# Kernel optimization log

Hardware: AMD Instinct MI355X
Metric: run time of the kernel (lower is better)

Reference implementation:

```python
import jax, jax.numpy as jnp
import numpy as np

N = 262144   # query points
M = 4096     # boundary points
D = 128      # d_model (m)
H = 4        # num_heads
HD = D // H  # head_dim = 32
L = 3        # num_layers
PI = float(np.pi)


def multi_feature_encoding(x):
    # x: [T, 2] -> [T, 30]; 15 fixed feature maps, hstacked
    feats = [
        x,
        x ** 2,
        (x - 1.5) ** 2,
        (x - 4.5) ** 2,
        jax.nn.sigmoid(x),
        jax.nn.sigmoid(x - 1.5),
        jax.nn.sigmoid(x - 4.5),
        x - 1.5,
        x - 4.5,
        jnp.sin(PI * x),
        jnp.cos(PI * x),
        jnp.sin(PI * x * 0.25),
        jnp.cos(PI * x * 0.25),
        jnp.sin(PI * x * 0.5),
        jnp.cos(PI * x * 0.5),
    ]
    return jnp.concatenate(feats, axis=-1)


def pos_encode(x, w, b):
    # w: [30, D], b: [D]
    return jnp.sin(multi_feature_encoding(x) @ w + b)


def setup_inputs() -> dict:
    key = jax.random.key(0)
    ks = jax.random.split(key, 24)
    s = 0.05

    def p(k, shape):
        return jax.random.normal(k, shape, dtype=jnp.float32) * s

    return {
        "query_pts": jax.random.normal(ks[0], (N, 2), dtype=jnp.float32),
        "boundary_pts": jax.random.normal(ks[1], (M, 2), dtype=jnp.float32),
        # positional encoders (query / boundary)
        "pe_w": p(ks[2], (30, D)), "pe_b": p(ks[3], (D,)),
        "bpe_w": p(ks[4], (30, D)), "bpe_b": p(ks[5], (D,)),
        # per-layer per-head q/k/v projections, stacked: [L, H, D, HD]
        "Wq": p(ks[6], (L, H, D, HD)), "bq": p(ks[7], (L, H, HD)),
        "Wk": p(ks[8], (L, H, D, HD)), "bk": p(ks[9], (L, H, HD)),
        "Wv": p(ks[10], (L, H, D, HD)), "bv": p(ks[11], (L, H, HD)),
        # attention out proj and FFN (two D->D linears) per layer
        "Wo": p(ks[12], (L, D, D)), "bo": p(ks[13], (L, D)),
        "W1": p(ks[14], (L, D, D)), "b1": p(ks[15], (L, D)),
        "W2": p(ks[16], (L, D, D)), "b2": p(ks[17], (L, D)),
        # final projector: D -> D//2 -> 3
        "pw1": p(ks[18], (D, D // 2)), "pb1": p(ks[19], (D // 2,)),
        "pw2": p(ks[20], (D // 2, 3)), "pb2": p(ks[21], (3,)),
    }


def reference(query_pts, boundary_pts, pe_w, pe_b, bpe_w, bpe_b,
              Wq, bq, Wk, bk, Wv, bv, Wo, bo, W1, b1, W2, b2,
              pw1, pb1, pw2, pb2):
    h = pos_encode(query_pts, pe_w, pe_b)[None]        # [1, N, D]
    b_enc = pos_encode(boundary_pts, bpe_w, bpe_b)[None]  # [1, M, D]

    for l in range(L):
        # batched per-head projections (equivalent to the per-head Linear loop)
        qh = jnp.einsum('btd,hde->bhte', h, Wq[l]) + bq[l][None, :, None, :]
        kh = jnp.einsum('btd,hde->bhte', b_enc, Wk[l]) + bk[l][None, :, None, :]
        vh = jnp.einsum('btd,hde->bhte', b_enc, Wv[l]) + bv[l][None, :, None, :]
        qh = qh ** 2  # squared feature map
        kh = kh ** 2
        kv_sum = jnp.einsum('bhnd,bhne->bhde', kh, vh)          # [1,H,HD,HD]
        z = 1.0 / (jnp.einsum('bhnd,bhd->bhn', qh, kh.sum(axis=2)) + 1e-6)
        attn = jnp.einsum('bhnd,bhde,bhn->bhne', qh, kv_sum, z)  # [1,H,N,HD]
        attn = attn.transpose(0, 2, 1, 3).reshape(1, -1, D)      # [1,N,D]
        attn = attn @ Wo[l] + bo[l]
        x = h + attn
        ff = jax.nn.gelu(x @ W1[l] + b1[l], approximate=False) @ W2[l] + b2[l]
        h = x + ff

    out = jax.nn.gelu(h @ pw1 + pb1, approximate=False) @ pw2 + pb2  # [1,N,3]
    return out[0]  # squeeze(0) -> [N, 3]
```

## Files before the change

### kernel.cpp

```cpp
#include <hip/hip_runtime.h>
#include <hip/hip_bf16.h>

__device__ __forceinline__ float b2f(unsigned short u) {
    return __uint_as_float(((unsigned)u) << 16);
}
__device__ __forceinline__ unsigned short f2b(float f) {
    __hip_bfloat16 h = __float2bfloat16(f);
    return *reinterpret_cast<unsigned short*>(&h);
}
__device__ __forceinline__ unsigned pk_bf16(float lo, float hi) {
    unsigned r;
    asm("v_cvt_pk_bf16_f32 %0, %1, %2" : "=v"(r) : "v"(lo), "v"(hi));
    return r;
}
__device__ __forceinline__ float exp2_hw(float x) {
    float r;
    asm("v_exp_f32 %0, %1" : "=v"(r) : "v"(x));
    return r;
}
__device__ __forceinline__ float sigm(float v) {
    return 1.f / (1.f + __expf(-v));
}
__device__ __forceinline__ float gelu_l(float x) {
    float x2 = x * x;
    float y  = x * __builtin_fmaf(0.10294535f, x2, 2.3022137f);
    float e  = exp2_hw(y);
    float r  = __builtin_amdgcn_rcpf(e + 1.f);
    return __builtin_fmaf(-x, r, x);
}

typedef __attribute__((ext_vector_type(8))) short s8v;
typedef __attribute__((ext_vector_type(4))) float f4v;

#define MFMA_BF16 __builtin_amdgcn_mfma_f32_16x16x32_bf16

__device__ __forceinline__ s8v mkfrag(unsigned a, unsigned b, unsigned c, unsigned d) {
    union { unsigned u[4]; s8v v; } x;
    x.u[0] = a; x.u[1] = b; x.u[2] = c; x.u[3] = d;
    return x.v;
}

__device__ __forceinline__ int fmap(int s) {
    return (s & ~31) | (((s >> 2) & 3) << 3) | (((s >> 4) & 1) << 2) | (s & 3);
}
__device__ __forceinline__ int swz_q(int q) {
    return q ^ (((q >> 7) & 7) << 3);
}

__device__ __forceinline__ void make_feats(const unsigned short* __restrict__ qpts,
                                           int r, float* __restrict__ f) {
    unsigned pq = *(const unsigned*)(qpts + (size_t)r * 2);
    float x0 = b2f((unsigned short)(pq & 0xffff));
    float x1 = b2f((unsigned short)(pq >> 16));
    const float PI = 3.14159265358979323846f;
    float a0 = x0 - 1.5f, a1 = x1 - 1.5f, c0 = x0 - 4.5f, c1 = x1 - 4.5f;
    f[0] = x0;        f[1] = x1;
    f[2] = x0 * x0;   f[3] = x1 * x1;
    f[4] = a0 * a0;   f[5] = a1 * a1;
    f[6] = c0 * c0;   f[7] = c1 * c1;
    f[8] = sigm(x0);  f[9] = sigm(x1);
    f[10] = sigm(a0); f[11] = sigm(a1);
    f[12] = sigm(c0); f[13] = sigm(c1);
    f[14] = a0;       f[15] = a1;
    f[16] = c0;       f[17] = c1;
    f[18] = __sinf(PI * x0);          f[19] = __sinf(PI * x1);
    f[20] = __cosf(PI * x0);          f[21] = __cosf(PI * x1);
    f[22] = __sinf(PI * 0.25f * x0);  f[23] = __sinf(PI * 0.25f * x1);
    f[24] = __cosf(PI * 0.25f * x0);  f[25] = __cosf(PI * 0.25f * x1);
    f[26] = __sinf(PI * 0.5f * x0);   f[27] = __sinf(PI * 0.5f * x1);
    f[28] = __cosf(PI * 0.5f * x0);   f[29] = __cosf(PI * 0.5f * x1);
}

__device__ __forceinline__ void feats8(unsigned pq, int qd, float* __restrict__ f8) {
    float x0 = b2f((unsigned short)(pq & 0xffff));
    float x1 = b2f((unsigned short)(pq >> 16));
    const float PI = 3.14159265358979323846f;
    float a0 = x0 - 1.5f, a1 = x1 - 1.5f, c0 = x0 - 4.5f, c1 = x1 - 4.5f;
    if (qd == 0) {
        f8[0] = x0;      f8[1] = x1;
        f8[2] = x0 * x0; f8[3] = x1 * x1;
        f8[4] = a0 * a0; f8[5] = a1 * a1;
        f8[6] = c0 * c0; f8[7] = c1 * c1;
    } else if (qd == 1) {
        f8[0] = sigm(x0); f8[1] = sigm(x1);
        f8[2] = sigm(a0); f8[3] = sigm(a1);
        f8[4] = sigm(c0); f8[5] = sigm(c1);
        f8[6] = a0;       f8[7] = a1;
    } else if (qd == 2) {
        f8[0] = c0; f8[1] = c1;
        f8[2] = __sinf(PI * x0);          f8[3] = __sinf(PI * x1);
        f8[4] = __cosf(PI * x0);          f8[5] = __cosf(PI * x1);
        f8[6] = __sinf(PI * 0.25f * x0);  f8[7] = __sinf(PI * 0.25f * x1);
    } else {
        f8[0] = __cosf(PI * 0.25f * x0);  f8[1] = __cosf(PI * 0.25f * x1);
        f8[2] = __sinf(PI * 0.5f * x0);   f8[3] = __sinf(PI * 0.5f * x1);
        f8[4] = __cosf(PI * 0.5f * x0);   f8[5] = __cosf(PI * 0.5f * x1);
        f8[6] = 0.f;                      f8[7] = 0.f;
    }
}

struct ConvArgs {
    const void* p[22];
    int off[23];
};

__global__ __launch_bounds__(256) void convert_kernel(
    ConvArgs a, const unsigned short* __restrict__ pe_w_raw,
    int* __restrict__ flag, unsigned short* __restrict__ canon, int total)
{
    __shared__ int cnt;
    if (threadIdx.x == 0) cnt = 0;
    __syncthreads();
    float v = b2f(pe_w_raw[threadIdx.x * 2]);
    if (!(fabsf(v) < 1.0f)) atomicAdd(&cnt, 1);
    __syncthreads();
    int isf32 = (cnt >= 16) ? 1 : 0;
    if (blockIdx.x == 0 && threadIdx.x == 0) *flag = isf32;

    int g = blockIdx.x * 256 + threadIdx.x;
    if (g >= total) return;
    int s = 0;
    #pragma unroll
    for (int i = 1; i < 23; i++) s += (g >= a.off[i]) ? 1 : 0;
    int local = g - a.off[s];
    unsigned short r;
    if (isf32) r = f2b(((const float*)a.p[s])[local]);
    else       r = ((const unsigned short*)a.p[s])[local];
    canon[g] = r;
}

__global__ __launch_bounds__(256) void encode_kernel(
    const unsigned short* __restrict__ pts,
    const unsigned short* __restrict__ w,
    const unsigned short* __restrict__ b,
    float* __restrict__ out)
{
    __shared__ __align__(16) float wsm[30 * 128];
    __shared__ float bs[128];
    int t = threadIdx.x;
    for (int i = t; i < 30 * 128; i += 256) wsm[i] = b2f(w[i]);
    if (t < 128) bs[t] = b2f(b[t]);
    __syncthreads();

    int r = blockIdx.x * 8 + (t >> 5);
    int j = t & 31;
    float f[30];
    make_feats(pts, r, f);
    float s0 = bs[j * 4 + 0], s1 = bs[j * 4 + 1], s2 = bs[j * 4 + 2], s3 = bs[j * 4 + 3];
    #pragma unroll
    for (int ff = 0; ff < 30; ff++) {
        float4 wv = *(const float4*)&wsm[ff * 128 + j * 4];
        float fv = f[ff];
        s0 += fv * wv.x; s1 += fv * wv.y; s2 += fv * wv.z; s3 += fv * wv.w;
    }
    *(float4*)&out[(size_t)r * 128 + j * 4] =
        make_float4(__sinf(s0), __sinf(s1), __sinf(s2), __sinf(s3));
}

__global__ __launch_bounds__(256) void khvh_kernel(
    const float* __restrict__ benc,
    const unsigned short* __restrict__ Wk, const unsigned short* __restrict__ bk,
    const unsigned short* __restrict__ Wv, const unsigned short* __restrict__ bv,
    float* __restrict__ kh, float* __restrict__ vh, float* __restrict__ kvz)
{
    int g = blockIdx.x * 256 + threadIdx.x;
    if (g < 12672) kvz[g] = 0.f;
    int lh = g >> 17;
    int rem = g & 131071;
    int m = rem >> 5;
    int dd = rem & 31;
    const unsigned short* wk = Wk + lh * 4096 + dd;
    const unsigned short* wv = Wv + lh * 4096 + dd;
    const float* br = benc + (size_t)m * 128;
    float ka = 0.f, va = 0.f;
    #pragma unroll 8
    for (int c = 0; c < 128; c++) {
        float bb = br[c];
        ka += bb * b2f(wk[c * 32]);
        va += bb * b2f(wv[c * 32]);
    }
    ka += b2f(bk[lh * 32 + dd]); ka = ka * ka;
    va += b2f(bv[lh * 32 + dd]);
    kh[g] = ka; vh[g] = va;
}

__global__ __launch_bounds__(1024) void kvred_kernel(
    const float* __restrict__ kh, const float* __restrict__ vh,
    float* __restrict__ kvsum, float* __restrict__ ksum)
{
    __shared__ float khs[1024];
    __shared__ float vhs[1024];
    int t = threadIdx.x;
    int lh = blockIdx.x >> 3;
    int part = blockIdx.x & 7;
    int dd = t >> 5, ee = t & 31;
    float kva = 0.f, ksa = 0.f;
    for (int ch = 0; ch < 16; ch++) {
        int base = lh * 131072 + (part * 16 + ch) * 1024;
        khs[t] = kh[base + t];
        vhs[t] = vh[base + t];
        __syncthreads();
        #pragma unroll
        for (int i = 0; i < 32; i++) {
            float kk = khs[i * 32 + dd];
            kva += kk * vhs[i * 32 + ee];
            ksa += kk;
        }
        __syncthreads();
    }
    atomicAdd(&kvsum[lh * 1024 + dd * 32 + ee], kva);
    if (ee == 0) atomicAdd(&ksum[lh * 32 + dd], ksa);
}

__global__ __launch_bounds__(256) void prep_kernel(
    const unsigned short* __restrict__ Wq, const unsigned short* __restrict__ W1,
    const unsigned short* __restrict__ W2, const unsigned short* __restrict__ pw1,
    const float* __restrict__ kvs, const float* __restrict__ kss,
    const unsigned short* __restrict__ Wo, const unsigned short* __restrict__ pe_w,
    unsigned short* __restrict__ wqT, unsigned short* __restrict__ w1T,
    unsigned short* __restrict__ w2T, unsigned short* __restrict__ pw1T,
    unsigned short* __restrict__ waT, unsigned short* __restrict__ ksT,
    unsigned short* __restrict__ pweT)
{
    int g = blockIdx.x * 256 + threadIdx.x;
    if (g < 49152) {
        int l = g >> 14, q = swz_q(g & 16383), n = q >> 7, k = q & 127;
        int na = fmap(n);
        wqT[g] = Wq[((l * 4 + (na >> 5)) * 128 + k) * 32 + (na & 31)];
    } else if (g < 98304) {
        int q0 = g - 49152; int l = q0 >> 14, q = swz_q(q0 & 16383), n = q >> 7, k = q & 127;
        w1T[q0] = W1[(l * 128 + k) * 128 + fmap(n)];
    } else if (g < 147456) {
        int q0 = g - 98304; int l = q0 >> 14, q = swz_q(q0 & 16383), n = q >> 7, k = q & 127;
        w2T[q0] = W2[(l * 128 + k) * 128 + fmap(n)];
    } else if (g < 155648) {
        int q0 = g - 147456; int q = swz_q(q0), n = q >> 7, k = q & 127;
        pw1T[q0] = pw1[k * 64 + n];
    } else if (g < 204800) {
        int q0 = g - 155648; int l = q0 >> 14, q = swz_q(q0 & 16383), n = q >> 7, k = q & 127;
        int na = fmap(n);
        int hk = k >> 5, dk = k & 31;
        const float* kvp = kvs + (l * 4 + hk) * 1024 + dk * 32;
        const unsigned short* wop = Wo + (size_t)(l * 128 + hk * 32) * 128 + na;
        float s = 0.f;
        #pragma unroll 8
        for (int j = 0; j < 32; j++) s += kvp[j] * b2f(wop[j * 128]);
        waT[q0] = f2b(s);
    } else if (g < 210944) {
        int q = g - 204800; int l = q >> 11, r = q & 2047, n = r >> 7, k = r & 127;
        unsigned short v = 0;
        if (n < 4 && (k >> 5) == n) v = f2b(kss[(l * 4 + n) * 32 + (k & 31)]);
        ksT[q] = v;
    } else if (g < 215040) {
        int q = g - 210944; int n = q >> 5, k = q & 31;
        pweT[q] = (k < 30) ? pe_w[k * 128 + fmap(n)] : (unsigned short)0;
    }
}


template<int ITERS>
__device__ __forceinline__ void stage_gll(const unsigned short* __restrict__ g,
                                          unsigned short* __restrict__ lbase,
                                          int wvi, int ln) {
    const char* gp = (const char*)g + wvi * 1024 + ln * 16;
    char* lp = (char*)lbase + wvi * 1024;
    #pragma unroll
    for (int i = 0; i < ITERS; i++) {
        __builtin_amdgcn_global_load_lds(
            (const __attribute__((address_space(1))) unsigned int*)(gp + i * 4096),
            (__attribute__((address_space(3))) unsigned int*)(lp + i * 4096),
            16, 0, 0);
    }
}

__device__ __forceinline__ s8v wfrag(const unsigned short* __restrict__ wb,
                                     int nt, int k, int l16, int qd) {
    int lin = (nt << 12) + (l16 << 8) + (k << 6) + (qd << 4);
    return *(const s8v*)((const char*)wb + (lin ^ ((l16 & 7) << 4)));
}

#define MM_BODY(WB, EPI...) do {                                              \
    s8v bf0[4], bf1[4];                                                       \
    _Pragma("unroll")                                                         \
    for (int _s = 0; _s < 4; _s++) {                                          \
        bf0[_s] = mkfrag(pkd[0][2*_s][0], pkd[0][2*_s][1],                    \
                         pkd[0][2*_s+1][0], pkd[0][2*_s+1][1]);               \
        bf1[_s] = mkfrag(pkd[1][2*_s][0], pkd[1][2*_s][1],                    \
                         pkd[1][2*_s+1][0], pkd[1][2*_s+1][1]);               \
    }                                                                         \
    _Pragma("unroll")                                                         \
    for (int _p = 0; _p < 4; _p++) {                                          \
        f4v _x0 = {0.f,0.f,0.f,0.f}, _x1 = _x0, _y0 = _x0, _y1 = _x0;         \
        _Pragma("unroll")                                                     \
        for (int _k = 0; _k < 4; _k++) {                                      \
            s8v _wa = wfrag(WB, _p * 2,     _k, l16, qd);                     \
            s8v _wb = wfrag(WB, _p * 2 + 1, _k, l16, qd);                     \
            _x0 = MFMA_BF16(_wa, bf0[_k], _x0, 0, 0, 0);                      \
            _x1 = MFMA_BF16(_wa, bf1[_k], _x1, 0, 0, 0);                      \
            _y0 = MFMA_BF16(_wb, bf0[_k], _y0, 0, 0, 0);                      \
            _y1 = MFMA_BF16(_wb, bf1[_k], _y1, 0, 0, 0);                      \
        }                                                                     \
        { const int nt = _p * 2;     const int tile = 0; const f4v x = _x0; EPI } \
        { const int nt = _p * 2;     const int tile = 1; const f4v x = _x1; EPI } \
        { const int nt = _p * 2 + 1; const int tile = 0; const f4v x = _y0; EPI } \
        { const int nt = _p * 2 + 1; const int tile = 1; const f4v x = _y1; EPI } \
    }                                                                         \
} while (0)

#define CBDEF int cb = ((nt >> 1) << 5) + (qd << 3) + ((nt & 1) << 2)

__global__ __launch_bounds__(256) void mega_kernel(
    const unsigned short* __restrict__ qpts,
    const unsigned short* __restrict__ pweT,
    const unsigned short* __restrict__ pe_b,
    const unsigned short* __restrict__ wqT,
    const unsigned short* __restrict__ waT,
    const unsigned short* __restrict__ ksT,
    const unsigned short* __restrict__ w1T,
    const unsigned short* __restrict__ w2T,
    const unsigned short* __restrict__ bq,
    const unsigned short* __restrict__ bo,
    const unsigned short* __restrict__ b1,
    const unsigned short* __restrict__ b2,
    const unsigned short* __restrict__ pw1T,
    const unsigned short* __restrict__ pb1,
    const unsigned short* __restrict__ pw2,
    const unsigned short* __restrict__ pb2,
    void* __restrict__ outv, const int* __restrict__ flag)
{
    __shared__ __align__(16) unsigned short wbuf[2][16384];
    __shared__ __align__(16) float biasAll[12 * 128];
    __shared__ __align__(16) float pebs[128];
    __shared__ __align__(16) float pb1s[64];
    __shared__ __align__(16) float w2s4[256];
    __shared__ float pb2s[3];

    int t = threadIdx.x;
    int wvi = t >> 6, ln = t & 63, qd = ln >> 4, l16 = ln & 15;
    int row0 = blockIdx.x * 128;
    int rA0 = wvi * 32 + l16;
    unsigned short* wb0 = &wbuf[0][0];
    unsigned short* wb1 = &wbuf[1][0];

    stage_gll<8>(wqT, wb0, wvi, ln);

    for (int i = t; i < 1536; i += 256) {
        int l = i >> 9, rem = i & 511, which = rem >> 7, c = rem & 127;
        const unsigned short* bsrc = (which == 0) ? bq : (which == 1) ? bo
                                   : (which == 2) ? b1 : b2;
        biasAll[i] = b2f(bsrc[l * 128 + c]);
    }
    if (t < 128) pebs[t] = b2f(pe_b[t]);
    if (t < 64)  pb1s[t] = b2f(pb1[t]);
    if (t < 64) {
        w2s4[t * 4 + 0] = b2f(pw2[t * 3 + 0]);
        w2s4[t * 4 + 1] = b2f(pw2[t * 3 + 1]);
        w2s4[t * 4 + 2] = b2f(pw2[t * 3 + 2]);
        w2s4[t * 4 + 3] = 0.f;
    }
    if (t < 3) pb2s[t] = b2f(pb2[t]);
    __syncthreads();

    stage_gll<8>(waT, wb1, wvi, ln);

    unsigned pkd[2][8][2];
    float hres[2][8][4];

    {
        unsigned pq0 = *(const unsigned*)(qpts + (size_t)(row0 + rA0) * 2);
        unsigned pq1 = *(const unsigned*)(qpts + (size_t)(row0 + rA0 + 16) * 2);
        s8v ae0, ae1;
        {
            float f8[8]; feats8(pq0, qd, f8);
            unsigned* au = (unsigned*)&ae0;
            #pragma unroll
            for (int jj = 0; jj < 4; jj++) au[jj] = pk_bf16(f8[2 * jj], f8[2 * jj + 1]);
        }
        {
            float f8[8]; feats8(pq1, qd, f8);
            unsigned* au = (unsigned*)&ae1;
            #pragma unroll
            for (int jj = 0; jj < 4; jj++) au[jj] = pk_bf16(f8[2 * jj], f8[2 * jj + 1]);
        }
        const unsigned short* pb = pweT + l16 * 32 + qd * 8;
        #pragma unroll
        for (int nt = 0; nt < 8; nt++) {
            s8v aw = *(const s8v*)(pb + nt * 512);
            f4v x0 = {0.f, 0.f, 0.f, 0.f}, x1 = {0.f, 0.f, 0.f, 0.f};
            x0 = MFMA_BF16(aw, ae0, x0, 0, 0, 0);
            x1 = MFMA_BF16(aw, ae1, x1, 0, 0, 0);
            CBDEF;
            float4 bb = *(const float4*)&pebs[cb];
            float h0 = __sinf(x0[0] + bb.x), h1 = __sinf(x0[1] + bb.y);
            float h2 = __sinf(x0[2] + bb.z), h3 = __sinf(x0[3] + bb.w);
            hres[0][nt][0] = h0; hres[0][nt][1] = h1;
            hres[0][nt][2] = h2; hres[0][nt][3] = h3;
            pkd[0][nt][0] = pk_bf16(h0, h1);
            pkd[0][nt][1] = pk_bf16(h2, h3);
            float g0 = __sinf(x1[0] + bb.x), g1 = __sinf(x1[1] + bb.y);
            float g2 = __sinf(x1[2] + bb.z), g3 = __sinf(x1[3] + bb.w);
            hres[1][nt][0] = g0; hres[1][nt][1] = g1;
            hres[1][nt][2] = g2; hres[1][nt][3] = g3;
            pkd[1][nt][0] = pk_bf16(g0, g1);
            pkd[1][nt][1] = pk_bf16(g2, g3);
        }
    }

    for (int l = 0; l < 3; l++) {
        const float* bql = &biasAll[(l * 4 + 0) * 128];
        const float* bol = &biasAll[(l * 4 + 1) * 128];
        const float* b1l = &biasAll[(l * 4 + 2) * 128];
        const float* b2l = &biasAll[(l * 4 + 3) * 128];

        s8v kf[4];
        {
            const unsigned short* kb = ksT + l * 2048 + l16 * 128 + qd * 8;
            #pragma unroll
            for (int ks = 0; ks < 4; ks++) kf[ks] = *(const s8v*)(kb + ks * 32);
        }

        MM_BODY(wb0, {
            CBDEF;
            float4 bb = *(const float4*)&bql[cb];
            float v0 = x[0] + bb.x, v1 = x[1] + bb.y;
            float v2 = x[2] + bb.z, v3 = x[3] + bb.w;
            pkd[tile][nt][0] = pk_bf16(v0 * v0, v1 * v1);
            pkd[tile][nt][1] = pk_bf16(v2 * v2, v3 * v3);
        });
        __syncthreads();
        stage_gll<8>(w1T + l * 16384, wb0, wvi, ln);

        #pragma unroll
        for (int tile = 0; tile < 2; tile++) {
            f4v d = {0.f, 0.f, 0.f, 0.f};
            #pragma unroll
            for (int ks = 0; ks < 4; ks++) {
                s8v b = mkfrag(pkd[tile][2 * ks][0], pkd[tile][2 * ks][1],
                               pkd[tile][2 * ks + 1][0], pkd[tile][2 * ks + 1][1]);
                d = MFMA_BF16(kf[ks], b, d, 0, 0, 0);
            }
            #pragma unroll
            for (int ks = 0; ks < 4; ks++) {
                float z = 1.f / (__shfl(d[ks], l16) + 1e-6f);
                #pragma unroll
                for (int h2 = 0; h2 < 2; h2++) {
                    #pragma unroll
                    for (int j = 0; j < 2; j++) {
                        unsigned w = pkd[tile][2 * ks + h2][j];
                        float lo = __uint_as_float(w << 16) * z;
                        float hi = __uint_as_float(w & 0xffff0000u) * z;
                        pkd[tile][2 * ks + h2][j] = pk_bf16(lo, hi);
                    }
                }
            }
        }

        MM_BODY(wb1, {
            CBDEF;
            float4 bb = *(const float4*)&bol[cb];
            float v0 = hres[tile][nt][0] + x[0] + bb.x;
            float v1 = hres[tile][nt][1] + x[1] + bb.y;
            float v2 = hres[tile][nt][2] + x[2] + bb.z;
            float v3 = hres[tile][nt][3] + x[3] + bb.w;
            hres[tile][nt][0] = v0; hres[tile][nt][1] = v1;
            hres[tile][nt][2] = v2; hres[tile][nt][3] = v3;
            pkd[tile][nt][0] = pk_bf16(v0, v1);
            pkd[tile][nt][1] = pk_bf16(v2, v3);
        });
        __syncthreads();
        stage_gll<8>(w2T + l * 16384, wb1, wvi, ln);

        MM_BODY(wb0, {
            CBDEF;
            float4 bb = *(const float4*)&b1l[cb];
            float g0 = gelu_l(x[0] + bb.x), g1 = gelu_l(x[1] + bb.y);
            float g2 = gelu_l(x[2] + bb.z), g3 = gelu_l(x[3] + bb.w);
            pkd[tile][nt][0] = pk_bf16(g0, g1);
            pkd[tile][nt][1] = pk_bf16(g2, g3);
        });
        __syncthreads();
        if (l < 2) stage_gll<8>(wqT + (l + 1) * 16384, wb0, wvi, ln);
        else       stage_gll<4>(pw1T, wb0, wvi, ln);

        MM_BODY(wb1, {
            CBDEF;
            float4 bb = *(const float4*)&b2l[cb];
            float v0 = hres[tile][nt][0] + x[0] + bb.x;
            float v1 = hres[tile][nt][1] + x[1] + bb.y;
            float v2 = hres[tile][nt][2] + x[2] + bb.z;
            float v3 = hres[tile][nt][3] + x[3] + bb.w;
            hres[tile][nt][0] = v0; hres[tile][nt][1] = v1;
            hres[tile][nt][2] = v2; hres[tile][nt][3] = v3;
            pkd[tile][nt][0] = pk_bf16(v0, v1);
            pkd[tile][nt][1] = pk_bf16(v2, v3);
        });
        __syncthreads();
        if (l < 2) stage_gll<8>(waT + (l + 1) * 16384, wb1, wvi, ln);
    }

    {
        s8v bf0[4], bf1[4];
        #pragma unroll
        for (int ks = 0; ks < 4; ks++) {
            bf0[ks] = mkfrag(pkd[0][2 * ks][0], pkd[0][2 * ks][1],
                             pkd[0][2 * ks + 1][0], pkd[0][2 * ks + 1][1]);
            bf1[ks] = mkfrag(pkd[1][2 * ks][0], pkd[1][2 * ks][1],
                             pkd[1][2 * ks + 1][0], pkd[1][2 * ks + 1][1]);
        }
        float pt0[3] = {0.f, 0.f, 0.f}, pt1[3] = {0.f, 0.f, 0.f};
        #pragma unroll
        for (int p = 0; p < 2; p++) {
            f4v y00 = {0.f,0.f,0.f,0.f}, y01 = y00, y10 = y00, y11 = y00;
            #pragma unroll
            for (int ks = 0; ks < 4; ks++) {
                s8v wa = wfrag(wb0, p * 2,     ks, l16, qd);
                s8v wb = wfrag(wb0, p * 2 + 1, ks, l16, qd);
                y00 = MFMA_BF16(wa, bf0[ks], y00, 0, 0, 0);
                y01 = MFMA_BF16(wa, bf1[ks], y01, 0, 0, 0);
                y10 = MFMA_BF16(wb, bf0[ks], y10, 0, 0, 0);
                y11 = MFMA_BF16(wb, bf1[ks], y11, 0, 0, 0);
            }
            #pragma unroll
            for (int e = 0; e < 2; e++) {
                int c0 = (p * 2 + e) * 16 + qd * 4;
                float4 bb = *(const float4*)&pb1s[c0];
                f4v ya = e ? y10 : y00;
                f4v yb = e ? y11 : y01;
                #pragma unroll
                for (int i = 0; i < 4; i++) {
                    float bbi = (i == 0) ? bb.x : (i == 1) ? bb.y : (i == 2) ? bb.z : bb.w;
                    float4 w = *(const float4*)&w2s4[(c0 + i) * 4];
                    float ga = gelu_l(ya[i] + bbi);
                    float gb = gelu_l(yb[i] + bbi);
                    pt0[0] = fmaf(ga, w.x, pt0[0]);
                    pt0[1] = fmaf(ga, w.y, pt0[1]);
                    pt0[2] = fmaf(ga, w.z, pt0[2]);
                    pt1[0] = fmaf(gb, w.x, pt1[0]);
                    pt1[1] = fmaf(gb, w.y, pt1[1]);
                    pt1[2] = fmaf(gb, w.z, pt1[2]);
                }
            }
        }
        #pragma unroll
        for (int c = 0; c < 3; c++) {
            pt0[c] += __shfl_xor(pt0[c], 16); pt0[c] += __shfl_xor(pt0[c], 32);
            pt1[c] += __shfl_xor(pt1[c], 16); pt1[c] += __shfl_xor(pt1[c], 32);
            pt0[c] += pb2s[c]; pt1[c] += pb2s[c];
        }
        if (ln < 16) {
            size_t r0 = (size_t)(row0 + rA0) * 3;
            size_t r1 = (size_t)(row0 + rA0 + 16) * 3;
            if (*flag) {
                float* o = (float*)outv;
                o[r0] = pt0[0]; o[r0 + 1] = pt0[1]; o[r0 + 2] = pt0[2];
                o[r1] = pt1[0]; o[r1 + 1] = pt1[1]; o[r1 + 2] = pt1[2];
            } else {
                unsigned short* o = (unsigned short*)outv;
                o[r0] = f2b(pt0[0]); o[r0 + 1] = f2b(pt0[1]); o[r0 + 2] = f2b(pt0[2]);
                o[r1] = f2b(pt1[0]); o[r1 + 1] = f2b(pt1[1]); o[r1 + 2] = f2b(pt1[2]);
            }
        }
    }
}

extern "C" void kernel_launch(void* const* d_in, const int* in_sizes, int n_in,
                              void* d_out, int out_size, void* d_ws, size_t ws_size,
                              hipStream_t stream) {
    const int N = in_sizes[0] / 2;
    const int M = in_sizes[1] / 2;

    ConvArgs ca;
    int total = 0;
    for (int i = 0; i < 22; i++) { ca.p[i] = d_in[i]; ca.off[i] = total; total += in_sizes[i]; }
    ca.off[22] = total;

    float* ws = (float*)d_ws;
    int* flag = (int*)ws;
    unsigned short* canon = (unsigned short*)(ws + 16);
    size_t canonF = ((size_t)(total + 1) / 2 + 15) & ~(size_t)15;
    float* b_enc = ws + 16 + canonF;
    float* khb   = b_enc + (size_t)M * 128;
    float* vhb   = khb + (size_t)12 * M * 32;
    float* kvs   = vhb + (size_t)12 * M * 32;
    float* kss   = kvs + 12288;
    unsigned short* wqT  = (unsigned short*)(kss + 384);
    unsigned short* waT  = wqT + 49152;
    unsigned short* w1T  = waT + 49152;
    unsigned short* w2T  = w1T + 49152;
    unsigned short* ksT  = w2T + 49152;
    unsigned short* pw1T = ksT + 6144;
    unsigned short* pweT = pw1T + 8192;

    const unsigned short* c_qpts = canon + ca.off[0];
    const unsigned short* c_bpts = canon + ca.off[1];
    const unsigned short* c_pew  = canon + ca.off[2];
    const unsigned short* c_peb  = canon + ca.off[3];
    const unsigned short* c_bpew = canon + ca.off[4];
    const unsigned short* c_bpeb = canon + ca.off[5];
    const unsigned short* c_Wq   = canon + ca.off[6];
    const unsigned short* c_bq   = canon + ca.off[7];
    const unsigned short* c_Wk   = canon + ca.off[8];
    const unsigned short* c_bk   = canon + ca.off[9];
    const unsigned short* c_Wv   = canon + ca.off[10];
    const unsigned short* c_bv   = canon + ca.off[11];
    const unsigned short* c_Wo   = canon + ca.off[12];
    const unsigned short* c_bo   = canon + ca.off[13];
    const unsigned short* c_W1   = canon + ca.off[14];
    const unsigned short* c_b1   = canon + ca.off[15];
    const unsigned short* c_W2   = canon + ca.off[16];
    const unsigned short* c_b2   = canon + ca.off[17];
    const unsigned short* c_pw1  = canon + ca.off[18];
    const unsigned short* c_pb1  = canon + ca.off[19];
    const unsigned short* c_pw2  = canon + ca.off[20];
    const unsigned short* c_pb2  = canon + ca.off[21];

    convert_kernel<<<(total + 255) / 256, 256, 0, stream>>>(
        ca, (const unsigned short*)d_in[2], flag, canon, total);

    encode_kernel<<<M / 8, 256, 0, stream>>>(c_bpts, c_bpew, c_bpeb, b_enc);
    khvh_kernel<<<(12 * M * 32) / 256, 256, 0, stream>>>(
        b_enc, c_Wk, c_bk, c_Wv, c_bv, khb, vhb, kvs);
    kvred_kernel<<<96, 1024, 0, stream>>>(khb, vhb, kvs, kss);
    prep_kernel<<<215040 / 256, 256, 0, stream>>>(
        c_Wq, c_W1, c_W2, c_pw1, kvs, kss, c_Wo, c_pew,
        wqT, w1T, w2T, pw1T, waT, ksT, pweT);

    mega_kernel<<<N / 128, 256, 0, stream>>>(
        c_qpts, pweT, c_peb, wqT, waT, ksT, w1T, w2T,
        c_bq, c_bo, c_b1, c_b2, pw1T, c_pb1, c_pw2, c_pb2, d_out, flag);
}
```

Before: 364.6 us.

## Split weight staging into half-matrix LDS buffers and pack residual math as float2

Weight matrices are now staged into LDS in two 8K-element halves. Each matmul's first half computes from one buffer while the other buffer holds the second half, so LDS use is halved, which allows more blocks per CU, and loads stream at finer granularity. Residual and bias epilogues use float2 vectors so the compiler can emit packed FP32 ops. The cost is twice as many barriers and a less overlapped prefetch distance, since each half is refilled right after use.

Result: no change. 357.4 us (-2.0%).

```diff
diff --git a/kernel.cpp b/kernel.cpp
--- a/kernel.cpp
+++ b/kernel.cpp
@@ -31,6 +31,7 @@
 
 typedef __attribute__((ext_vector_type(8))) short s8v;
 typedef __attribute__((ext_vector_type(4))) float f4v;
+typedef __attribute__((ext_vector_type(2))) float f2v;
 
 #define MFMA_BF16 __builtin_amdgcn_mfma_f32_16x16x32_bf16
 
@@ -274,13 +275,12 @@
 }
 
 __device__ __forceinline__ s8v wfrag(const unsigned short* __restrict__ wb,
-                                     int nt, int k, int l16, int qd) {
-    int lin = (nt << 12) + (l16 << 8) + (k << 6) + (qd << 4);
+                                     int ntl, int k, int l16, int qd) {
+    int lin = (ntl << 12) + (l16 << 8) + (k << 6) + (qd << 4);
     return *(const s8v*)((const char*)wb + (lin ^ ((l16 & 7) << 4)));
 }
 
-#define MM_BODY(WB, EPI...) do {                                              \
-    s8v bf0[4], bf1[4];                                                       \
+#define CAPTURE() do {                                                        \
     _Pragma("unroll")                                                         \
     for (int _s = 0; _s < 4; _s++) {                                          \
         bf0[_s] = mkfrag(pkd[0][2*_s][0], pkd[0][2*_s][1],                    \
@@ -288,13 +288,17 @@
         bf1[_s] = mkfrag(pkd[1][2*_s][0], pkd[1][2*_s][1],                    \
                          pkd[1][2*_s+1][0], pkd[1][2*_s+1][1]);               \
     }                                                                         \
+} while (0)
+
+#define MM_HALF(WB, PB, EPI...) do {                                          \
     _Pragma("unroll")                                                         \
-    for (int _p = 0; _p < 4; _p++) {                                          \
+    for (int _pp = 0; _pp < 2; _pp++) {                                       \
+        const int _p = (PB) + _pp;                                            \
         f4v _x0 = {0.f,0.f,0.f,0.f}, _x1 = _x0, _y0 = _x0, _y1 = _x0;         \
         _Pragma("unroll")                                                     \
         for (int _k = 0; _k < 4; _k++) {                                      \
-            s8v _wa = wfrag(WB, _p * 2,     _k, l16, qd);                     \
-            s8v _wb = wfrag(WB, _p * 2 + 1, _k, l16, qd);                     \
+            s8v _wa = wfrag(WB, (_p * 2) & 3,     _k, l16, qd);               \
+            s8v _wb = wfrag(WB, (_p * 2 + 1) & 3, _k, l16, qd);               \
             _x0 = MFMA_BF16(_wa, bf0[_k], _x0, 0, 0, 0);                      \
             _x1 = MFMA_BF16(_wa, bf1[_k], _x1, 0, 0, 0);                      \
             _y0 = MFMA_BF16(_wb, bf0[_k], _y0, 0, 0, 0);                      \
@@ -328,7 +332,7 @@
     const unsigned short* __restrict__ pb2,
     void* __restrict__ outv, const int* __restrict__ flag)
 {
-    __shared__ __align__(16) unsigned short wbuf[2][16384];
+    __shared__ __align__(16) unsigned short wbuf[2][8192];
     __shared__ __align__(16) float biasAll[12 * 128];
     __shared__ __align__(16) float pebs[128];
     __shared__ __align__(16) float pb1s[64];
@@ -342,7 +346,7 @@
     unsigned short* wb0 = &wbuf[0][0];
     unsigned short* wb1 = &wbuf[1][0];
 
-    stage_gll<8>(wqT, wb0, wvi, ln);
+    stage_gll<4>(wqT, wb0, wvi, ln);
 
     for (int i = t; i < 1536; i += 256) {
         int l = i >> 9, rem = i & 511, which = rem >> 7, c = rem & 127;
@@ -361,10 +365,10 @@
     if (t < 3) pb2s[t] = b2f(pb2[t]);
     __syncthreads();
 
-    stage_gll<8>(waT, wb1, wvi, ln);
+    stage_gll<4>(wqT + 8192, wb1, wvi, ln);
 
     unsigned pkd[2][8][2];
-    float hres[2][8][4];
+    f2v hresv[2][8][2];
 
     {
         unsigned pq0 = *(const unsigned*)(qpts + (size_t)(row0 + rA0) * 2);
@@ -393,17 +397,49 @@
             float4 bb = *(const float4*)&pebs[cb];
             float h0 = __sinf(x0[0] + bb.x), h1 = __sinf(x0[1] + bb.y);
             float h2 = __sinf(x0[2] + bb.z), h3 = __sinf(x0[3] + bb.w);
-            hres[0][nt][0] = h0; hres[0][nt][1] = h1;
-            hres[0][nt][2] = h2; hres[0][nt][3] = h3;
+            f2v ha = {h0, h1}, hb = {h2, h3};
+            hresv[0][nt][0] = ha; hresv[0][nt][1] = hb;
             pkd[0][nt][0] = pk_bf16(h0, h1);
             pkd[0][nt][1] = pk_bf16(h2, h3);
             float g0 = __sinf(x1[0] + bb.x), g1 = __sinf(x1[1] + bb.y);
             float g2 = __sinf(x1[2] + bb.z), g3 = __sinf(x1[3] + bb.w);
-            hres[1][nt][0] = g0; hres[1][nt][1] = g1;
-            hres[1][nt][2] = g2; hres[1][nt][3] = g3;
+            f2v ga = {g0, g1}, gb = {g2, g3};
+            hresv[1][nt][0] = ga; hresv[1][nt][1] = gb;
             pkd[1][nt][0] = pk_bf16(g0, g1);
             pkd[1][nt][1] = pk_bf16(g2, g3);
         }
+    }
+
+    s8v bf0[4], bf1[4];
+
+    #define EPI_MM1 {                                                         \
+        CBDEF;                                                                \
+        float4 bb = *(const float4*)&bql[cb];                                 \
+        f2v xa = {x[0], x[1]}, xb = {x[2], x[3]};                             \
+        f2v ba = {bb.x, bb.y}, bc = {bb.z, bb.w};                             \
+        f2v va = xa + ba, vb = xb + bc;                                       \
+        f2v sa = va * va, sb = vb * vb;                                       \
+        pkd[tile][nt][0] = pk_bf16(sa[0], sa[1]);                             \
+        pkd[tile][nt][1] = pk_bf16(sb[0], sb[1]);                             \
+    }
+    #define EPI_RES(BIAS) {                                                   \
+        CBDEF;                                                                \
+        float4 bb = *(const float4*)&BIAS[cb];                                \
+        f2v xa = {x[0], x[1]}, xb = {x[2], x[3]};                             \
+        f2v ba = {bb.x, bb.y}, bc = {bb.z, bb.w};                             \
+        f2v va = hresv[tile][nt][0] + xa + ba;                                \
+        f2v vb = hresv[tile][nt][1] + xb + bc;                                \
+        hresv[tile][nt][0] = va; hresv[tile][nt][1] = vb;                     \
+        pkd[tile][nt][0] = pk_bf16(va[0], va[1]);                             \
+        pkd[tile][nt][1] = pk_bf16(vb[0], vb[1]);                             \
+    }
+    #define EPI_GELU {                                                        \
+        CBDEF;                                                                \
+        float4 bb = *(const float4*)&b1l[cb];                                 \
+        float g0 = gelu_l(x[0] + bb.x), g1 = gelu_l(x[1] + bb.y);             \
+        float g2 = gelu_l(x[2] + bb.z), g3 = gelu_l(x[3] + bb.w);             \
+        pkd[tile][nt][0] = pk_bf16(g0, g1);                                   \
+        pkd[tile][nt][1] = pk_bf16(g2, g3);                                   \
     }
 
     for (int l = 0; l < 3; l++) {
@@ -419,16 +455,13 @@
             for (int ks = 0; ks < 4; ks++) kf[ks] = *(const s8v*)(kb + ks * 32);
         }
 
-        MM_BODY(wb0, {
-            CBDEF;
-            float4 bb = *(const float4*)&bql[cb];
-            float v0 = x[0] + bb.x, v1 = x[1] + bb.y;
-            float v2 = x[2] + bb.z, v3 = x[3] + bb.w;
-            pkd[tile][nt][0] = pk_bf16(v0 * v0, v1 * v1);
-            pkd[tile][nt][1] = pk_bf16(v2 * v2, v3 * v3);
-        });
-        __syncthreads();
-        stage_gll<8>(w1T + l * 16384, wb0, wvi, ln);
+        CAPTURE();
+        MM_HALF(wb0, 0, EPI_MM1);
+        __syncthreads();
+        stage_gll<4>(waT + l * 16384, wb0, wvi, ln);
+        MM_HALF(wb1, 2, EPI_MM1);
+        __syncthreads();
+        stage_gll<4>(waT + l * 16384 + 8192, wb1, wvi, ln);
 
         #pragma unroll
         for (int tile = 0; tile < 2; tile++) {
@@ -455,58 +488,34 @@
             }
         }
 
-        MM_BODY(wb1, {
-            CBDEF;
-            float4 bb = *(const float4*)&bol[cb];
-            float v0 = hres[tile][nt][0] + x[0] + bb.x;
-            float v1 = hres[tile][nt][1] + x[1] + bb.y;
-            float v2 = hres[tile][nt][2] + x[2] + bb.z;
-            float v3 = hres[tile][nt][3] + x[3] + bb.w;
-            hres[tile][nt][0] = v0; hres[tile][nt][1] = v1;
-            hres[tile][nt][2] = v2; hres[tile][nt][3] = v3;
-            pkd[tile][nt][0] = pk_bf16(v0, v1);
-            pkd[tile][nt][1] = pk_bf16(v2, v3);
-        });
-        __syncthreads();
-        stage_gll<8>(w2T + l * 16384, wb1, wvi, ln);
-
-        MM_BODY(wb0, {
-            CBDEF;
-            float4 bb = *(const float4*)&b1l[cb];
-            float g0 = gelu_l(x[0] + bb.x), g1 = gelu_l(x[1] + bb.y);
-            float g2 = gelu_l(x[2] + bb.z), g3 = gelu_l(x[3] + bb.w);
-            pkd[tile][nt][0] = pk_bf16(g0, g1);
-            pkd[tile][nt][1] = pk_bf16(g2, g3);
-        });
-        __syncthreads();
-        if (l < 2) stage_gll<8>(wqT + (l + 1) * 16384, wb0, wvi, ln);
+        CAPTURE();
+        MM_HALF(wb0, 0, EPI_RES(bol));
+        __syncthreads();
+        stage_gll<4>(w1T + l * 16384, wb0, wvi, ln);
+        MM_HALF(wb1, 2, EPI_RES(bol));
+        __syncthreads();
+        stage_gll<4>(w1T + l * 16384 + 8192, wb1, wvi, ln);
+
+        CAPTURE();
+        MM_HALF(wb0, 0, EPI_GELU);
+        __syncthreads();
+        stage_gll<4>(w2T + l * 16384, wb0, wvi, ln);
+        MM_HALF(wb1, 2, EPI_GELU);
+        __syncthreads();
+        stage_gll<4>(w2T + l * 16384 + 8192, wb1, wvi, ln);
+
+        CAPTURE();
+        MM_HALF(wb0, 0, EPI_RES(b2l));
+        __syncthreads();
+        if (l < 2) stage_gll<4>(wqT + (l + 1) * 16384, wb0, wvi, ln);
         else       stage_gll<4>(pw1T, wb0, wvi, ln);
-
-        MM_BODY(wb1, {
-            CBDEF;
-            float4 bb = *(const float4*)&b2l[cb];
-            float v0 = hres[tile][nt][0] + x[0] + bb.x;
-            float v1 = hres[tile][nt][1] + x[1] + bb.y;
-            float v2 = hres[tile][nt][2] + x[2] + bb.z;
-            float v3 = hres[tile][nt][3] + x[3] + bb.w;
-            hres[tile][nt][0] = v0; hres[tile][nt][1] = v1;
-            hres[tile][nt][2] = v2; hres[tile][nt][3] = v3;
-            pkd[tile][nt][0] = pk_bf16(v0, v1);
-            pkd[tile][nt][1] = pk_bf16(v2, v3);
-        });
-        __syncthreads();
-        if (l < 2) stage_gll<8>(waT + (l + 1) * 16384, wb1, wvi, ln);
+        MM_HALF(wb1, 2, EPI_RES(b2l));
+        __syncthreads();
+        if (l < 2) stage_gll<4>(wqT + (l + 1) * 16384 + 8192, wb1, wvi, ln);
     }
 
     {
-        s8v bf0[4], bf1[4];
-        #pragma unroll
-        for (int ks = 0; ks < 4; ks++) {
-            bf0[ks] = mkfrag(pkd[0][2 * ks][0], pkd[0][2 * ks][1],
-                             pkd[0][2 * ks + 1][0], pkd[0][2 * ks + 1][1]);
-            bf1[ks] = mkfrag(pkd[1][2 * ks][0], pkd[1][2 * ks][1],
-                             pkd[1][2 * ks + 1][0], pkd[1][2 * ks + 1][1]);
-        }
+        CAPTURE();
         float pt0[3] = {0.f, 0.f, 0.f}, pt1[3] = {0.f, 0.f, 0.f};
         #pragma unroll
         for (int p = 0; p < 2; p++) {
```
